# Performance work log

Measured on AMD Instinct MI355X. Metric: run time of the kernel, lower is better.

Reference implementation:

```python
import jax, jax.numpy as jnp
import numpy as np


def setup_inputs() -> dict:
    key = jax.random.key(0)
    k1, k2, k3 = jax.random.split(key, 3)
    B, L, H, E = 2, 2048, 16, 64
    queries = jax.random.normal(k1, (B, L, H, E), dtype=jnp.float32)
    keys = jax.random.normal(k2, (B, L, H, E), dtype=jnp.float32)
    values = jax.random.normal(k3, (B, L, H, E), dtype=jnp.float32)
    a1 = jnp.ones((), dtype=jnp.float32)
    a2 = jnp.ones((), dtype=jnp.float32)
    return {"queries": queries, "keys": keys, "values": values, "a1": a1, "a2": a2}


def reference(queries, keys, values, a1, a2):
    # ASSAAttention forward (eval mode: dropout is identity)
    B, L, H, E = queries.shape
    scale = 1.0 / jnp.sqrt(jnp.asarray(E, queries.dtype))
    # shared QK scores: [B, H, L, S]
    qk_scores = jnp.einsum('blhe,bshe->bhls', queries, keys) * scale
    # sparse path: squared-ReLU weighting
    ssa_scores = jax.nn.relu(qk_scores) ** 2
    ssa_output = jnp.einsum('bhls,bshd->blhd', ssa_scores, values)
    # dense path: softmax weighting
    dsa_scores = jax.nn.softmax(qk_scores, axis=-1)
    dsa_output = jnp.einsum('bhls,bshd->blhd', dsa_scores, values)
    # scalar blend with softmax over (a1, a2)
    w1 = jnp.exp(a1)
    w2 = jnp.exp(a2)
    alpha1 = w1 / (w1 + w2)
    alpha2 = w2 / (w1 + w2)
    return alpha1 * ssa_output + alpha2 * dsa_output
```

## Files before the change

### kernel.cpp

```cpp
#include <hip/hip_runtime.h>
#include <hip/hip_bf16.h>

typedef __attribute__((ext_vector_type(8))) short short8;
typedef __attribute__((ext_vector_type(4))) float f32x4;
typedef __attribute__((ext_vector_type(2))) float f32x2;
typedef __attribute__((ext_vector_type(4))) unsigned uint4v;

#define LOG2E 1.4426950408889634f
#define ILN2SQ 0.4804530139182014f

__device__ __forceinline__ unsigned packbf2(float a, float b) {
  __hip_bfloat162 h = __float22bfloat162_rn(make_float2(a, b));
  return *reinterpret_cast<unsigned*>(&h);
}
__device__ __forceinline__ int swz(int row) {
  return ((row & 7) << 4) ^ (((row >> 3) & 3) << 5);
}
__device__ __forceinline__ void gload16(const void* g, void* l) {
  __builtin_amdgcn_global_load_lds(
      (const __attribute__((address_space(1))) unsigned int*)g,
      (__attribute__((address_space(3))) unsigned int*)l, 16, 0, 0);
}

__device__ __forceinline__ int pv_key(int p) {
  const int R = p >> 5, g = (p & 31) >> 3, jj = p & 7;
  return (R * 2 + (jj >> 2)) * 16 + g * 4 + (jj & 3);
}

__global__ __launch_bounds__(256) void assa_prep(
    const float* __restrict__ K, const float* __restrict__ V, char* __restrict__ WS)
{
  constexpr int L = 2048, RS = 1024, E = 64;
  char* KP = WS;
  char* VTP = WS + (size_t)8 * 1024 * 1024;
  __shared__ float tile[64][65];
  const int tid = threadIdx.x;

  if (blockIdx.x < 1024) {
    const int gid = blockIdx.x * 256 + tid;
    const int rid = gid >> 2;
    const int e0 = (gid & 3) * 16;
    const int bh = rid >> 11, s = rid & 2047;
    const int b = bh >> 4, h = bh & 15;
    const float* kr = K + ((size_t)b * L + s) * RS + h * E + e0;
    const float4 u0 = *(const float4*)(kr);
    const float4 u1 = *(const float4*)(kr + 4);
    const float4 u2 = *(const float4*)(kr + 8);
    const float4 u3 = *(const float4*)(kr + 12);
    uint4v w0, w1;
    w0[0] = packbf2(u0.x, u0.y); w0[1] = packbf2(u0.z, u0.w);
    w0[2] = packbf2(u1.x, u1.y); w0[3] = packbf2(u1.z, u1.w);
    w1[0] = packbf2(u2.x, u2.y); w1[1] = packbf2(u2.z, u2.w);
    w1[2] = packbf2(u3.x, u3.y); w1[3] = packbf2(u3.z, u3.w);
    char* dst = KP + (size_t)rid * 128;
    const int sz = swz(s);
    *(uint4v*)(dst + ((e0 * 2) ^ sz)) = w0;
    *(uint4v*)(dst + ((e0 * 2 + 16) ^ sz)) = w1;
  } else {
    const int bx = blockIdx.x - 1024;
    const int bh = bx >> 5, t5 = bx & 31;
    const int b = bh >> 4, h = bh & 15;
    const float* vb = V + ((size_t)b * L + t5 * 64) * RS + h * E;
    {
      const int key = tid >> 2, e0 = (tid & 3) * 16;
      const float* vr = vb + (size_t)key * RS + e0;
      const float4 u0 = *(const float4*)(vr);
      const float4 u1 = *(const float4*)(vr + 4);
      const float4 u2 = *(const float4*)(vr + 8);
      const float4 u3 = *(const float4*)(vr + 12);
      float* tr = &tile[key][e0];
      tr[0] = u0.x; tr[1] = u0.y; tr[2] = u0.z; tr[3] = u0.w;
      tr[4] = u1.x; tr[5] = u1.y; tr[6] = u1.z; tr[7] = u1.w;
      tr[8] = u2.x; tr[9] = u2.y; tr[10] = u2.z; tr[11] = u2.w;
      tr[12] = u3.x; tr[13] = u3.y; tr[14] = u3.z; tr[15] = u3.w;
    }
    __syncthreads();
    const int e = tid >> 2, p0 = (tid & 3) * 16;
    uint4v w0, w1;
    #pragma unroll
    for (int i = 0; i < 4; ++i)
      w0[i] = packbf2(tile[pv_key(p0 + 2 * i)][e], tile[pv_key(p0 + 2 * i + 1)][e]);
    #pragma unroll
    for (int i = 0; i < 4; ++i)
      w1[i] = packbf2(tile[pv_key(p0 + 8 + 2 * i)][e], tile[pv_key(p0 + 9 + 2 * i)][e]);
    char* dst = VTP + ((size_t)bx * 64 + e) * 128;
    const int sz = swz(e);
    *(uint4v*)(dst + ((p0 * 2) ^ sz)) = w0;
    *(uint4v*)(dst + ((p0 * 2 + 16) ^ sz)) = w1;
  }
}

__global__ __launch_bounds__(512, 2) void assa_fused(
    const float* __restrict__ Q, const char* __restrict__ WS,
    const float* __restrict__ A1, const float* __restrict__ A2,
    float* __restrict__ O)
{
  constexpr int L = 2048, H = 16, E = 64, RS = H * E;

  __shared__ __align__(16) char Kb[2 * 16384];
  __shared__ __align__(16) char Vb[2 * 16384];

  const int t = threadIdx.x;
  const int wv = t >> 6;
  const int lane = t & 63;
  const int g = lane >> 4;
  const int c = lane & 15;

  const int bh = blockIdx.x;
  const int q0 = blockIdx.y * 128;
  const int b = bh >> 4;
  const int h = bh & 15;

  const float* qb = Q + (size_t)b * L * RS + (size_t)h * E;
  float* ob = O + (size_t)b * L * RS + (size_t)h * E;
  const char* KP = WS;
  const char* VTP = WS + (size_t)8 * 1024 * 1024;

  const float a1 = A1[0], a2 = A2[0];
  const float am = fmaxf(a1, a2);
  const float e1 = expf(a1 - am), e2 = expf(a2 - am);
  const float alpha1 = (e1 / (e1 + e2)) * ILN2SQ;
  const float alpha2 = e2 / (e1 + e2);

  short8 aq[2];
  {
    const float qs = 0.125f * LOG2E;
    const float* qr = qb + (size_t)(q0 + wv * 16 + c) * RS;
    #pragma unroll
    for (int ks = 0; ks < 2; ++ks) {
      const float4 u0 = *(const float4*)(qr + ks * 32 + g * 8);
      const float4 u1 = *(const float4*)(qr + ks * 32 + g * 8 + 4);
      union { unsigned u[4]; short8 s; } f;
      f.u[0] = packbf2(u0.x * qs, u0.y * qs);
      f.u[1] = packbf2(u0.z * qs, u0.w * qs);
      f.u[2] = packbf2(u1.x * qs, u1.y * qs);
      f.u[3] = packbf2(u1.z * qs, u1.w * qs);
      aq[ks] = f.s;
    }
  }

  int ka[8];
  #pragma unroll
  for (int i16 = 0; i16 < 4; ++i16) {
    const int row = i16 * 16 + c;
    const int s = swz(row);
    ka[i16 * 2 + 0] = (row * 128 + g * 16) ^ s;
    ka[i16 * 2 + 1] = (row * 128 + 64 + g * 16) ^ s;
  }

  const f32x4 zero4 = {0.0f, 0.0f, 0.0f, 0.0f};
  f32x4 od[4], os[4];
  #pragma unroll
  for (int i = 0; i < 4; ++i) { od[i] = zero4; os[i] = zero4; }
  f32x2 psa = {0.0f, 0.0f}, psb = {0.0f, 0.0f};

  const char* kp = KP + (size_t)bh * (2048 * 128) + t * 16;
  const char* vp = VTP + (size_t)bh * (2048 * 128) + t * 16;
  char* kd = Kb + wv * 1024;
  char* vd = Vb + wv * 1024;

  union U8 { unsigned u[4]; short8 s; };

#define STAGE(TOFF, HALF)                                \
  do {                                                   \
    gload16(kp + (TOFF), kd + (HALF));                   \
    gload16(kp + (TOFF) + 8192, kd + (HALF) + 8192);     \
    gload16(vp + (TOFF), vd + (HALF));                   \
    gload16(vp + (TOFF) + 8192, vd + (HALF) + 8192);     \
  } while (0)

#define QKPART(ACC, OFS)                                                             \
  do {                                                                               \
    _Pragma("unroll")                                                                \
    for (int kt = 0; kt < 4; ++kt) {                                                 \
      const short8 kf0 = *(const short8*)(Kb + ka[kt * 2 + 0] + (OFS));              \
      const short8 kf1 = *(const short8*)(Kb + ka[kt * 2 + 1] + (OFS));              \
      ACC[kt] = __builtin_amdgcn_mfma_f32_16x16x32_bf16(kf0, aq[0], ACC[kt], 0, 0, 0);\
      ACC[kt] = __builtin_amdgcn_mfma_f32_16x16x32_bf16(kf1, aq[1], ACC[kt], 0, 0, 0);\
    }                                                                                \
  } while (0)

#define SMPV(ACC, OFS)                                                               \
  do {                                                                               \
    _Pragma("unroll")                                                                \
    for (int tp = 0; tp < 2; ++tp) {                                                 \
      short8 vfA0 = *(const short8*)(Vb + ka[0 * 2 + tp] + (OFS));                   \
      short8 vfA1 = *(const short8*)(Vb + ka[1 * 2 + tp] + (OFS));                   \
      short8 vfA2 = *(const short8*)(Vb + ka[2 * 2 + tp] + (OFS));                   \
      short8 vfA3 = *(const short8*)(Vb + ka[3 * 2 + tp] + (OFS));                   \
      const f32x4 a0 = ACC[tp * 2], a1 = ACC[tp * 2 + 1];                            \
      const float x00 = __builtin_amdgcn_exp2f(a0[0]);                               \
      const float x01 = __builtin_amdgcn_exp2f(a0[1]);                               \
      const float x02 = __builtin_amdgcn_exp2f(a0[2]);                               \
      const float x03 = __builtin_amdgcn_exp2f(a0[3]);                               \
      const float x10 = __builtin_amdgcn_exp2f(a1[0]);                               \
      const float x11 = __builtin_amdgcn_exp2f(a1[1]);                               \
      const float x12 = __builtin_amdgcn_exp2f(a1[2]);                               \
      const float x13 = __builtin_amdgcn_exp2f(a1[3]);                               \
      psa += (f32x2){x00, x01}; psb += (f32x2){x02, x03};                            \
      psa += (f32x2){x10, x11}; psb += (f32x2){x12, x13};                            \
      f32x2 r00 = {a0[0], a0[1]}, r01 = {a0[2], a0[3]};                              \
      f32x2 r10 = {a1[0], a1[1]}, r11 = {a1[2], a1[3]};                              \
      const f32x2 z2 = {0.0f, 0.0f};                                                 \
      r00 = __builtin_elementwise_max(r00, z2); r00 *= r00;                          \
      r01 = __builtin_elementwise_max(r01, z2); r01 *= r01;                          \
      r10 = __builtin_elementwise_max(r10, z2); r10 *= r10;                          \
      r11 = __builtin_elementwise_max(r11, z2); r11 *= r11;                          \
      U8 bpd, bps;                                                                   \
      bpd.u[0] = packbf2(x00, x01); bpd.u[1] = packbf2(x02, x03);                    \
      bpd.u[2] = packbf2(x10, x11); bpd.u[3] = packbf2(x12, x13);                    \
      bps.u[0] = packbf2(r00[0], r00[1]); bps.u[1] = packbf2(r01[0], r01[1]);        \
      bps.u[2] = packbf2(r10[0], r10[1]); bps.u[3] = packbf2(r11[0], r11[1]);        \
      __builtin_amdgcn_s_setprio(1);                                                 \
      od[0] = __builtin_amdgcn_mfma_f32_16x16x32_bf16(vfA0, bpd.s, od[0], 0, 0, 0);  \
      os[0] = __builtin_amdgcn_mfma_f32_16x16x32_bf16(vfA0, bps.s, os[0], 0, 0, 0);  \
      od[1] = __builtin_amdgcn_mfma_f32_16x16x32_bf16(vfA1, bpd.s, od[1], 0, 0, 0);  \
      os[1] = __builtin_amdgcn_mfma_f32_16x16x32_bf16(vfA1, bps.s, os[1], 0, 0, 0);  \
      od[2] = __builtin_amdgcn_mfma_f32_16x16x32_bf16(vfA2, bpd.s, od[2], 0, 0, 0);  \
      os[2] = __builtin_amdgcn_mfma_f32_16x16x32_bf16(vfA2, bps.s, os[2], 0, 0, 0);  \
      od[3] = __builtin_amdgcn_mfma_f32_16x16x32_bf16(vfA3, bpd.s, od[3], 0, 0, 0);  \
      os[3] = __builtin_amdgcn_mfma_f32_16x16x32_bf16(vfA3, bps.s, os[3], 0, 0, 0);  \
      __builtin_amdgcn_s_setprio(0);                                                 \
    }                                                                                \
  } while (0)

#define SUBTILE(SOFF)                                    \
  do {                                                   \
    f32x4 acc[4];                                        \
    _Pragma("unroll")                                    \
    for (int i = 0; i < 4; ++i) acc[i] = zero4;          \
    QKPART(acc, SOFF);                                   \
    SMPV(acc, SOFF);                                     \
  } while (0)

  STAGE(0, 0);
  __syncthreads();
  int toff = 16384;
  for (int r = 0; r < 16; ++r) {
    if (r + 1 < 16) { STAGE(toff, ((r + 1) & 1) * 16384); toff += 16384; }
    const int OFS = (r & 1) * 16384;
    SUBTILE(OFS);
    SUBTILE(OFS + 8192);
    __syncthreads();
  }
#undef STAGE
#undef QKPART
#undef SMPV
#undef SUBTILE

  const f32x2 lv = psa + psb;
  float l = lv[0] + lv[1];
  l += __shfl_xor(l, 16);
  l += __shfl_xor(l, 32);

  const float wd = alpha2 / l;
  float* orow = ob + (size_t)(q0 + wv * 16 + c) * RS;
  #pragma unroll
  for (int et = 0; et < 4; ++et) {
    float4 o;
    o.x = alpha1 * os[et][0] + wd * od[et][0];
    o.y = alpha1 * os[et][1] + wd * od[et][1];
    o.z = alpha1 * os[et][2] + wd * od[et][2];
    o.w = alpha1 * os[et][3] + wd * od[et][3];
    *(float4*)(orow + et * 16 + g * 4) = o;
  }
}

extern "C" void kernel_launch(void* const* d_in, const int* in_sizes, int n_in,
                              void* d_out, int out_size, void* d_ws, size_t ws_size,
                              hipStream_t stream) {
  const float* q = (const float*)d_in[0];
  const float* k = (const float*)d_in[1];
  const float* v = (const float*)d_in[2];
  const float* a1 = (const float*)d_in[3];
  const float* a2 = (const float*)d_in[4];
  float* out = (float*)d_out;
  char* ws = (char*)d_ws;

  assa_prep<<<2048, 256, 0, stream>>>(k, v, ws);
  dim3 grid(32, 16);
  assa_fused<<<grid, 512, 0, stream>>>(q, ws, a1, a2, out);
}
```

Before: 80.18 us.

## Switch attention MFMAs to 32x32x16 tiles with four waves of 32 queries

Replaces the 16x16x32 bf16 MFMA tiling with 32x32x16 MFMAs. Each of four waves now owns 32 query rows, so the block shrinks from 512 to 256 threads while still covering 128 queries. The V-transpose permutation in the prep kernel is reworked to match the new operand layout, and staging uses four 16-byte loads per thread. The aim is fewer MFMA issues and LDS fragment reads per FLOP, at the cost of fewer waves per block for hiding latency and higher per-wave register pressure from the 16-wide accumulators.

```diff
diff --git a/kernel.cpp b/kernel.cpp
--- a/kernel.cpp
+++ b/kernel.cpp
@@ -2,7 +2,7 @@
 #include <hip/hip_bf16.h>
 
 typedef __attribute__((ext_vector_type(8))) short short8;
-typedef __attribute__((ext_vector_type(4))) float f32x4;
+typedef __attribute__((ext_vector_type(16))) float f32x16;
 typedef __attribute__((ext_vector_type(2))) float f32x2;
 typedef __attribute__((ext_vector_type(4))) unsigned uint4v;
 
@@ -22,9 +22,10 @@
       (__attribute__((address_space(3))) unsigned int*)l, 16, 0, 0);
 }
 
-__device__ __forceinline__ int pv_key(int p) {
-  const int R = p >> 5, g = (p & 31) >> 3, jj = p & 7;
-  return (R * 2 + (jj >> 2)) * 16 + g * 4 + (jj & 3);
+__device__ __forceinline__ int pv_key32(int p) {
+  const int s = p >> 4, T = s >> 1, sg = s & 1;
+  const int h = (p & 15) >> 3, idx = p & 7;
+  return 32 * T + 16 * sg + 4 * h + (idx < 4 ? idx : idx + 4);
 }
 
 __global__ __launch_bounds__(256) void assa_prep(
@@ -79,10 +80,10 @@
     uint4v w0, w1;
     #pragma unroll
     for (int i = 0; i < 4; ++i)
-      w0[i] = packbf2(tile[pv_key(p0 + 2 * i)][e], tile[pv_key(p0 + 2 * i + 1)][e]);
+      w0[i] = packbf2(tile[pv_key32(p0 + 2 * i)][e], tile[pv_key32(p0 + 2 * i + 1)][e]);
     #pragma unroll
     for (int i = 0; i < 4; ++i)
-      w1[i] = packbf2(tile[pv_key(p0 + 8 + 2 * i)][e], tile[pv_key(p0 + 9 + 2 * i)][e]);
+      w1[i] = packbf2(tile[pv_key32(p0 + 8 + 2 * i)][e], tile[pv_key32(p0 + 9 + 2 * i)][e]);
     char* dst = VTP + ((size_t)bx * 64 + e) * 128;
     const int sz = swz(e);
     *(uint4v*)(dst + ((p0 * 2) ^ sz)) = w0;
@@ -90,7 +91,7 @@
   }
 }
 
-__global__ __launch_bounds__(512, 2) void assa_fused(
+__global__ __launch_bounds__(256, 2) void assa_fused(
     const float* __restrict__ Q, const char* __restrict__ WS,
     const float* __restrict__ A1, const float* __restrict__ A2,
     float* __restrict__ O)
@@ -103,16 +104,16 @@
   const int t = threadIdx.x;
   const int wv = t >> 6;
   const int lane = t & 63;
-  const int g = lane >> 4;
-  const int c = lane & 15;
+  const int cq = lane & 31;
+  const int h = lane >> 5;
 
   const int bh = blockIdx.x;
   const int q0 = blockIdx.y * 128;
   const int b = bh >> 4;
-  const int h = bh & 15;
-
-  const float* qb = Q + (size_t)b * L * RS + (size_t)h * E;
-  float* ob = O + (size_t)b * L * RS + (size_t)h * E;
+  const int hh = bh & 15;
+
+  const float* qb = Q + (size_t)b * L * RS + (size_t)hh * E;
+  float* ob = O + (size_t)b * L * RS + (size_t)hh * E;
   const char* KP = WS;
   const char* VTP = WS + (size_t)8 * 1024 * 1024;
 
@@ -122,36 +123,36 @@
   const float alpha1 = (e1 / (e1 + e2)) * ILN2SQ;
   const float alpha2 = e2 / (e1 + e2);
 
-  short8 aq[2];
+  short8 aq[4];
   {
     const float qs = 0.125f * LOG2E;
-    const float* qr = qb + (size_t)(q0 + wv * 16 + c) * RS;
-    #pragma unroll
-    for (int ks = 0; ks < 2; ++ks) {
-      const float4 u0 = *(const float4*)(qr + ks * 32 + g * 8);
-      const float4 u1 = *(const float4*)(qr + ks * 32 + g * 8 + 4);
+    const float* qr = qb + (size_t)(q0 + wv * 32 + cq) * RS;
+    #pragma unroll
+    for (int kk = 0; kk < 4; ++kk) {
+      const float4 u0 = *(const float4*)(qr + kk * 16 + h * 8);
+      const float4 u1 = *(const float4*)(qr + kk * 16 + h * 8 + 4);
       union { unsigned u[4]; short8 s; } f;
       f.u[0] = packbf2(u0.x * qs, u0.y * qs);
       f.u[1] = packbf2(u0.z * qs, u0.w * qs);
       f.u[2] = packbf2(u1.x * qs, u1.y * qs);
       f.u[3] = packbf2(u1.z * qs, u1.w * qs);
-      aq[ks] = f.s;
+      aq[kk] = f.s;
     }
   }
 
   int ka[8];
   #pragma unroll
-  for (int i16 = 0; i16 < 4; ++i16) {
-    const int row = i16 * 16 + c;
+  for (int i = 0; i < 2; ++i) {
+    const int row = i * 32 + cq;
     const int s = swz(row);
-    ka[i16 * 2 + 0] = (row * 128 + g * 16) ^ s;
-    ka[i16 * 2 + 1] = (row * 128 + 64 + g * 16) ^ s;
-  }
-
-  const f32x4 zero4 = {0.0f, 0.0f, 0.0f, 0.0f};
-  f32x4 od[4], os[4];
+    #pragma unroll
+    for (int j = 0; j < 4; ++j)
+      ka[i * 4 + j] = row * 128 + ((32 * j + 16 * h) ^ s);
+  }
+
+  f32x16 od0, od1, os0, os1;
   #pragma unroll
-  for (int i = 0; i < 4; ++i) { od[i] = zero4; os[i] = zero4; }
+  for (int i = 0; i < 16; ++i) { od0[i] = 0.0f; od1[i] = 0.0f; os0[i] = 0.0f; os1[i] = 0.0f; }
   f32x2 psa = {0.0f, 0.0f}, psb = {0.0f, 0.0f};
 
   const char* kp = KP + (size_t)bh * (2048 * 128) + t * 16;
@@ -161,76 +162,67 @@
 
   union U8 { unsigned u[4]; short8 s; };
 
-#define STAGE(TOFF, HALF)                                \
-  do {                                                   \
-    gload16(kp + (TOFF), kd + (HALF));                   \
-    gload16(kp + (TOFF) + 8192, kd + (HALF) + 8192);     \
-    gload16(vp + (TOFF), vd + (HALF));                   \
-    gload16(vp + (TOFF) + 8192, vd + (HALF) + 8192);     \
+#define STAGE(TOFF, HALF)                                        \
+  do {                                                           \
+    _Pragma("unroll")                                            \
+    for (int j = 0; j < 4; ++j) {                                \
+      gload16(kp + (TOFF) + j * 4096, kd + (HALF) + j * 4096);   \
+      gload16(vp + (TOFF) + j * 4096, vd + (HALF) + j * 4096);   \
+    }                                                            \
   } while (0)
 
-#define QKPART(ACC, OFS)                                                             \
+#define SLICE(ACCT, SG, S, OFS)                                                      \
   do {                                                                               \
+    const short8 vf0 = *(const short8*)(Vb + ka[0 * 4 + (S)] + (OFS));               \
+    const short8 vf1 = *(const short8*)(Vb + ka[1 * 4 + (S)] + (OFS));               \
+    const float x0 = __builtin_amdgcn_exp2f(ACCT[8 * (SG) + 0]);                     \
+    const float x1 = __builtin_amdgcn_exp2f(ACCT[8 * (SG) + 1]);                     \
+    const float x2 = __builtin_amdgcn_exp2f(ACCT[8 * (SG) + 2]);                     \
+    const float x3 = __builtin_amdgcn_exp2f(ACCT[8 * (SG) + 3]);                     \
+    const float x4 = __builtin_amdgcn_exp2f(ACCT[8 * (SG) + 4]);                     \
+    const float x5 = __builtin_amdgcn_exp2f(ACCT[8 * (SG) + 5]);                     \
+    const float x6 = __builtin_amdgcn_exp2f(ACCT[8 * (SG) + 6]);                     \
+    const float x7 = __builtin_amdgcn_exp2f(ACCT[8 * (SG) + 7]);                     \
+    psa += (f32x2){x0, x1}; psb += (f32x2){x2, x3};                                  \
+    psa += (f32x2){x4, x5}; psb += (f32x2){x6, x7};                                  \
+    f32x2 r0 = {ACCT[8 * (SG) + 0], ACCT[8 * (SG) + 1]};                             \
+    f32x2 r1 = {ACCT[8 * (SG) + 2], ACCT[8 * (SG) + 3]};                             \
+    f32x2 r2 = {ACCT[8 * (SG) + 4], ACCT[8 * (SG) + 5]};                             \
+    f32x2 r3 = {ACCT[8 * (SG) + 6], ACCT[8 * (SG) + 7]};                             \
+    const f32x2 z2 = {0.0f, 0.0f};                                                   \
+    r0 = __builtin_elementwise_max(r0, z2); r0 *= r0;                                \
+    r1 = __builtin_elementwise_max(r1, z2); r1 *= r1;                                \
+    r2 = __builtin_elementwise_max(r2, z2); r2 *= r2;                                \
+    r3 = __builtin_elementwise_max(r3, z2); r3 *= r3;                                \
+    U8 bpd, bps;                                                                     \
+    bpd.u[0] = packbf2(x0, x1); bpd.u[1] = packbf2(x2, x3);                          \
+    bpd.u[2] = packbf2(x4, x5); bpd.u[3] = packbf2(x6, x7);                          \
+    bps.u[0] = packbf2(r0[0], r0[1]); bps.u[1] = packbf2(r1[0], r1[1]);              \
+    bps.u[2] = packbf2(r2[0], r2[1]); bps.u[3] = packbf2(r3[0], r3[1]);              \
+    __builtin_amdgcn_s_setprio(1);                                                   \
+    od0 = __builtin_amdgcn_mfma_f32_32x32x16_bf16(vf0, bpd.s, od0, 0, 0, 0);         \
+    os0 = __builtin_amdgcn_mfma_f32_32x32x16_bf16(vf0, bps.s, os0, 0, 0, 0);         \
+    od1 = __builtin_amdgcn_mfma_f32_32x32x16_bf16(vf1, bpd.s, od1, 0, 0, 0);         \
+    os1 = __builtin_amdgcn_mfma_f32_32x32x16_bf16(vf1, bps.s, os1, 0, 0, 0);         \
+    __builtin_amdgcn_s_setprio(0);                                                   \
+  } while (0)
+
+#define SUBTILE(OFS)                                                                 \
+  do {                                                                               \
+    f32x16 acc0, acc1;                                                               \
     _Pragma("unroll")                                                                \
-    for (int kt = 0; kt < 4; ++kt) {                                                 \
-      const short8 kf0 = *(const short8*)(Kb + ka[kt * 2 + 0] + (OFS));              \
-      const short8 kf1 = *(const short8*)(Kb + ka[kt * 2 + 1] + (OFS));              \
-      ACC[kt] = __builtin_amdgcn_mfma_f32_16x16x32_bf16(kf0, aq[0], ACC[kt], 0, 0, 0);\
-      ACC[kt] = __builtin_amdgcn_mfma_f32_16x16x32_bf16(kf1, aq[1], ACC[kt], 0, 0, 0);\
+    for (int i = 0; i < 16; ++i) { acc0[i] = 0.0f; acc1[i] = 0.0f; }                 \
+    _Pragma("unroll")                                                                \
+    for (int kk = 0; kk < 4; ++kk) {                                                 \
+      const short8 kf0 = *(const short8*)(Kb + ka[0 * 4 + kk] + (OFS));              \
+      const short8 kf1 = *(const short8*)(Kb + ka[1 * 4 + kk] + (OFS));              \
+      acc0 = __builtin_amdgcn_mfma_f32_32x32x16_bf16(kf0, aq[kk], acc0, 0, 0, 0);    \
+      acc1 = __builtin_amdgcn_mfma_f32_32x32x16_bf16(kf1, aq[kk], acc1, 0, 0, 0);    \
     }                                                                                \
-  } while (0)
-
-#define SMPV(ACC, OFS)                                                               \
-  do {                                                                               \
-    _Pragma("unroll")                                                                \
-    for (int tp = 0; tp < 2; ++tp) {                                                 \
-      short8 vfA0 = *(const short8*)(Vb + ka[0 * 2 + tp] + (OFS));                   \
-      short8 vfA1 = *(const short8*)(Vb + ka[1 * 2 + tp] + (OFS));                   \
-      short8 vfA2 = *(const short8*)(Vb + ka[2 * 2 + tp] + (OFS));                   \
-      short8 vfA3 = *(const short8*)(Vb + ka[3 * 2 + tp] + (OFS));                   \
-      const f32x4 a0 = ACC[tp * 2], a1 = ACC[tp * 2 + 1];                            \
-      const float x00 = __builtin_amdgcn_exp2f(a0[0]);                               \
-      const float x01 = __builtin_amdgcn_exp2f(a0[1]);                               \
-      const float x02 = __builtin_amdgcn_exp2f(a0[2]);                               \
-      const float x03 = __builtin_amdgcn_exp2f(a0[3]);                               \
-      const float x10 = __builtin_amdgcn_exp2f(a1[0]);                               \
-      const float x11 = __builtin_amdgcn_exp2f(a1[1]);                               \
-      const float x12 = __builtin_amdgcn_exp2f(a1[2]);                               \
-      const float x13 = __builtin_amdgcn_exp2f(a1[3]);                               \
-      psa += (f32x2){x00, x01}; psb += (f32x2){x02, x03};                            \
-      psa += (f32x2){x10, x11}; psb += (f32x2){x12, x13};                            \
-      f32x2 r00 = {a0[0], a0[1]}, r01 = {a0[2], a0[3]};                              \
-      f32x2 r10 = {a1[0], a1[1]}, r11 = {a1[2], a1[3]};                              \
-      const f32x2 z2 = {0.0f, 0.0f};                                                 \
-      r00 = __builtin_elementwise_max(r00, z2); r00 *= r00;                          \
-      r01 = __builtin_elementwise_max(r01, z2); r01 *= r01;                          \
-      r10 = __builtin_elementwise_max(r10, z2); r10 *= r10;                          \
-      r11 = __builtin_elementwise_max(r11, z2); r11 *= r11;                          \
-      U8 bpd, bps;                                                                   \
-      bpd.u[0] = packbf2(x00, x01); bpd.u[1] = packbf2(x02, x03);                    \
-      bpd.u[2] = packbf2(x10, x11); bpd.u[3] = packbf2(x12, x13);                    \
-      bps.u[0] = packbf2(r00[0], r00[1]); bps.u[1] = packbf2(r01[0], r01[1]);        \
-      bps.u[2] = packbf2(r10[0], r10[1]); bps.u[3] = packbf2(r11[0], r11[1]);        \
-      __builtin_amdgcn_s_setprio(1);                                                 \
-      od[0] = __builtin_amdgcn_mfma_f32_16x16x32_bf16(vfA0, bpd.s, od[0], 0, 0, 0);  \
-      os[0] = __builtin_amdgcn_mfma_f32_16x16x32_bf16(vfA0, bps.s, os[0], 0, 0, 0);  \
-      od[1] = __builtin_amdgcn_mfma_f32_16x16x32_bf16(vfA1, bpd.s, od[1], 0, 0, 0);  \
-      os[1] = __builtin_amdgcn_mfma_f32_16x16x32_bf16(vfA1, bps.s, os[1], 0, 0, 0);  \
-      od[2] = __builtin_amdgcn_mfma_f32_16x16x32_bf16(vfA2, bpd.s, od[2], 0, 0, 0);  \
-      os[2] = __builtin_amdgcn_mfma_f32_16x16x32_bf16(vfA2, bps.s, os[2], 0, 0, 0);  \
-      od[3] = __builtin_amdgcn_mfma_f32_16x16x32_bf16(vfA3, bpd.s, od[3], 0, 0, 0);  \
-      os[3] = __builtin_amdgcn_mfma_f32_16x16x32_bf16(vfA3, bps.s, os[3], 0, 0, 0);  \
-      __builtin_amdgcn_s_setprio(0);                                                 \
-    }                                                                                \
-  } while (0)
-
-#define SUBTILE(SOFF)                                    \
-  do {                                                   \
-    f32x4 acc[4];                                        \
-    _Pragma("unroll")                                    \
-    for (int i = 0; i < 4; ++i) acc[i] = zero4;          \
-    QKPART(acc, SOFF);                                   \
-    SMPV(acc, SOFF);                                     \
+    SLICE(acc0, 0, 0, OFS);                                                          \
+    SLICE(acc0, 1, 1, OFS);                                                          \
+    SLICE(acc1, 0, 2, OFS);                                                          \
+    SLICE(acc1, 1, 3, OFS);                                                          \
   } while (0)
 
   STAGE(0, 0);
@@ -244,25 +236,28 @@
     __syncthreads();
   }
 #undef STAGE
-#undef QKPART
-#undef SMPV
+#undef SLICE
 #undef SUBTILE
 
   const f32x2 lv = psa + psb;
   float l = lv[0] + lv[1];
-  l += __shfl_xor(l, 16);
   l += __shfl_xor(l, 32);
 
   const float wd = alpha2 / l;
-  float* orow = ob + (size_t)(q0 + wv * 16 + c) * RS;
+  float* orow = ob + (size_t)(q0 + wv * 32 + cq) * RS;
   #pragma unroll
-  for (int et = 0; et < 4; ++et) {
-    float4 o;
-    o.x = alpha1 * os[et][0] + wd * od[et][0];
-    o.y = alpha1 * os[et][1] + wd * od[et][1];
-    o.z = alpha1 * os[et][2] + wd * od[et][2];
-    o.w = alpha1 * os[et][3] + wd * od[et][3];
-    *(float4*)(orow + et * 16 + g * 4) = o;
+  for (int rq = 0; rq < 4; ++rq) {
+    float4 o0, o1;
+    o0.x = alpha1 * os0[4 * rq + 0] + wd * od0[4 * rq + 0];
+    o0.y = alpha1 * os0[4 * rq + 1] + wd * od0[4 * rq + 1];
+    o0.z = alpha1 * os0[4 * rq + 2] + wd * od0[4 * rq + 2];
+    o0.w = alpha1 * os0[4 * rq + 3] + wd * od0[4 * rq + 3];
+    o1.x = alpha1 * os1[4 * rq + 0] + wd * od1[4 * rq + 0];
+    o1.y = alpha1 * os1[4 * rq + 1] + wd * od1[4 * rq + 1];
+    o1.z = alpha1 * os1[4 * rq + 2] + wd * od1[4 * rq + 2];
+    o1.w = alpha1 * os1[4 * rq + 3] + wd * od1[4 * rq + 3];
+    *(float4*)(orow + 8 * rq + 4 * h) = o0;
+    *(float4*)(orow + 32 + 8 * rq + 4 * h) = o1;
   }
 }
 
@@ -279,5 +274,5 @@
 
   assa_prep<<<2048, 256, 0, stream>>>(k, v, ws);
   dim3 grid(32, 16);
-  assa_fused<<<grid, 512, 0, stream>>>(q, ws, a1, a2, out);
-}
+  assa_fused<<<grid, 256, 0, stream>>>(q, ws, a1, a2, out);
+}
```

Measured after the change: 78.80 us. No clear change (-1.7%).
